# Kernel tuning notes

Measured on AMD Instinct MI355X. Metric: run time of the kernel, lower is better.

## Reference

```python
import jax, jax.numpy as jnp
import numpy as np
from jax import lax

SMOOTH = 1e-06
SKEL_ITERS = 10  # thresh_width in the original soft_skeletonize


def _maxpool3(x):
    # 3x3 max pool, stride 1, padding 1 on NCHW
    return lax.reduce_window(
        x, -jnp.inf, lax.max,
        window_dimensions=(1, 1, 3, 3),
        window_strides=(1, 1, 1, 1),
        padding=((0, 0), (0, 0), (1, 1), (1, 1)))


def soft_skeletonize(x):
    def body(i, x):
        min_pool_x = -_maxpool3(-x)                      # 3x3 min-pool (erosion)
        contour = jax.nn.relu(_maxpool3(min_pool_x) - min_pool_x)
        return jax.nn.relu(x - contour)
    return lax.fori_loop(0, SKEL_ITERS, body, x)


def norm_intersection(center_line, vessel):
    B, C = center_line.shape[:2]
    clf = center_line.reshape(B, C, -1)
    vf = vessel.reshape(B, C, -1)
    intersection = jnp.sum(clf * vf, axis=-1)
    return (intersection + SMOOTH) / (jnp.sum(clf, axis=-1) + SMOOTH)


def setup_inputs() -> dict:
    key = jax.random.key(0)
    k1, k2 = jax.random.split(key)
    B, C, H, W = 32, 1, 512, 512
    pred = jax.random.uniform(k1, (B, C, H, W), dtype=jnp.float32)
    target = (jax.random.uniform(k2, (B, C, H, W), dtype=jnp.float32) > 0.85).astype(jnp.float32)
    return {"pred": pred, "target": target}


def reference(pred, target):
    cl_pred = soft_skeletonize(pred)
    target_skeleton = soft_skeletonize(target)
    iflat = norm_intersection(cl_pred, target)
    tflat = norm_intersection(target_skeleton, pred)
    intersection = jnp.sum(iflat * tflat)
    return 1.0 - 2.0 * intersection / jnp.sum(iflat + tflat)
```

## Files before the change

kernel.cpp:

```cpp
#include <hip/hip_runtime.h>
#include <math.h>

#define HH 512
#define WW 512
#define BB 32
#define CHUNK 32

__device__ __forceinline__ float min3f(float a, float b, float c) {
    return fminf(fminf(a, b), c);
}
__device__ __forceinline__ float max3f(float a, float b, float c) {
    return fmaxf(fmaxf(a, b), c);
}
__device__ __forceinline__ float bf2f(unsigned short h) {
    return __uint_as_float((unsigned)h << 16);
}
__device__ __forceinline__ unsigned short f2bf(float f) {
    unsigned u = __float_as_uint(f);
    u += 0x7FFF + ((u >> 16) & 1);
    return (unsigned short)(u >> 16);
}

template <int F32>
__device__ __forceinline__ void loadrow12(const float* __restrict__ imgF,
                                          const unsigned short* __restrict__ imgH,
                                          int R, int cm4, int c0, int cp4,
                                          bool isL, bool isR, float* xr) {
    const int Rc = R < 0 ? 0 : (R > HH - 1 ? HH - 1 : R);
    if (F32) {
        const float* rb = imgF + (size_t)Rc * WW;
        float4 v0 = *(const float4*)(rb + cm4);
        float4 v1 = *(const float4*)(rb + c0);
        float4 v2 = *(const float4*)(rb + cp4);
        xr[0] = v0.x; xr[1] = v0.y; xr[2] = v0.z; xr[3] = v0.w;
        xr[4] = v1.x; xr[5] = v1.y; xr[6] = v1.z; xr[7] = v1.w;
        xr[8] = v2.x; xr[9] = v2.y; xr[10] = v2.z; xr[11] = v2.w;
    } else {
        const unsigned short* rb = imgH + (size_t)Rc * WW;
        ushort4 v0 = *(const ushort4*)(rb + cm4);
        ushort4 v1 = *(const ushort4*)(rb + c0);
        ushort4 v2 = *(const ushort4*)(rb + cp4);
        xr[0] = bf2f(v0.x); xr[1] = bf2f(v0.y); xr[2] = bf2f(v0.z); xr[3] = bf2f(v0.w);
        xr[4] = bf2f(v1.x); xr[5] = bf2f(v1.y); xr[6] = bf2f(v1.z); xr[7] = bf2f(v1.w);
        xr[8] = bf2f(v2.x); xr[9] = bf2f(v2.y); xr[10] = bf2f(v2.z); xr[11] = bf2f(v2.w);
    }
    if (isL) xr[3] = xr[0];
    if (isR) xr[8] = xr[7];
}

template <int SRCF32, int FUSED>
__device__ __forceinline__ void rowstep(
    const float* __restrict__ imgF, const unsigned short* __restrict__ imgH,
    const float* __restrict__ cmp, unsigned short* __restrict__ outp,
    float& acc0, float& acc1,
    int R, int cm4, int gx0, int cp4, bool isL, bool isR, bool doStore,
    float (&xA)[12], float (&xL)[12],
    float (&hm0o)[10], float (&hm0n)[10], float (&mn0p)[8],
    float (&hx0o)[8], float (&hx0n)[8],
    float (&x0o)[8], float (&x0n)[8],
    float (&hm1o)[6], float (&hm1n)[6], float (&mn1p)[4],
    float (&hx1o)[4], float (&hx1n)[4],
    float (&x1o)[4], float (&x1n)[4],
    float4& cqC, float4& cqL) {
    loadrow12<SRCF32>(imgF, imgH, R + 3, cm4, gx0, cp4, isL, isR, xL);

    float4 cmpCur;
    if (FUSED) {
        cmpCur = cqC;
        int Rc = R - 1;
        Rc = Rc < 0 ? 0 : (Rc > HH - 1 ? HH - 1 : Rc);
        cqL = *(const float4*)(cmp + (size_t)Rc * WW + gx0);
    }

    float hm0c[10];
    #pragma unroll
    for (int i = 0; i < 10; ++i) hm0c[i] = min3f(xA[i], xA[i + 1], xA[i + 2]);

    float mn0n[10];
    #pragma unroll
    for (int i = 0; i < 10; ++i) mn0n[i] = min3f(hm0o[i], hm0n[i], hm0c[i]);
    if (!((unsigned)(R - 1) < HH)) {
        #pragma unroll
        for (int i = 0; i < 10; ++i) mn0n[i] = -INFINITY;
    }
    if (isL) { mn0n[0] = -INFINITY; mn0n[1] = -INFINITY; mn0n[2] = -INFINITY; }
    if (isR) { mn0n[7] = -INFINITY; mn0n[8] = -INFINITY; mn0n[9] = -INFINITY; }

    float hx0c[8];
    #pragma unroll
    for (int j = 0; j < 8; ++j) hx0c[j] = max3f(mn0n[j], mn0n[j + 1], mn0n[j + 2]);

    float x1c[8];
    #pragma unroll
    for (int j = 0; j < 8; ++j) {
        float mp = max3f(hx0o[j], hx0n[j], hx0c[j]);
        float ct = fmaxf(mp - mn0p[j], 0.0f);
        x1c[j] = fmaxf(x0o[j] - ct, 0.0f);
    }
    if (!((unsigned)(R - 2) < HH)) {
        #pragma unroll
        for (int j = 0; j < 8; ++j) x1c[j] = INFINITY;
    }
    if (isL) { x1c[0] = INFINITY; x1c[1] = INFINITY; }
    if (isR) { x1c[6] = INFINITY; x1c[7] = INFINITY; }

    #pragma unroll
    for (int i = 0; i < 10; ++i) hm0o[i] = hm0c[i];
    #pragma unroll
    for (int j = 0; j < 8; ++j) { mn0p[j] = mn0n[j + 1]; hx0o[j] = hx0c[j]; x0o[j] = xA[j + 2]; }

    float hm1c[6];
    #pragma unroll
    for (int k = 0; k < 6; ++k) hm1c[k] = min3f(x1c[k], x1c[k + 1], x1c[k + 2]);

    float mn1n[6];
    #pragma unroll
    for (int k = 0; k < 6; ++k) mn1n[k] = min3f(hm1o[k], hm1n[k], hm1c[k]);
    if (!((unsigned)(R - 3) < HH)) {
        #pragma unroll
        for (int k = 0; k < 6; ++k) mn1n[k] = -INFINITY;
    }
    if (isL) mn1n[0] = -INFINITY;
    if (isR) mn1n[5] = -INFINITY;

    float hx1c[4];
    #pragma unroll
    for (int m = 0; m < 4; ++m) hx1c[m] = max3f(mn1n[m], mn1n[m + 1], mn1n[m + 2]);

    if (doStore) {
        float o[4];
        #pragma unroll
        for (int m = 0; m < 4; ++m) {
            float mp = max3f(hx1o[m], hx1n[m], hx1c[m]);
            float ct = fmaxf(mp - mn1p[m], 0.0f);
            o[m] = fmaxf(x1o[m] - ct, 0.0f);
        }
        if (FUSED) {
            acc0 += o[0] * cmpCur.x + o[1] * cmpCur.y + o[2] * cmpCur.z + o[3] * cmpCur.w;
            acc1 += o[0] + o[1] + o[2] + o[3];
        } else {
            ushort4 ov;
            ov.x = f2bf(o[0]); ov.y = f2bf(o[1]); ov.z = f2bf(o[2]); ov.w = f2bf(o[3]);
            *(ushort4*)(outp + (size_t)(R - 4) * WW + gx0) = ov;
        }
    }

    #pragma unroll
    for (int k = 0; k < 6; ++k) hm1o[k] = hm1c[k];
    #pragma unroll
    for (int m = 0; m < 4; ++m) { mn1p[m] = mn1n[m + 1]; hx1o[m] = hx1c[m]; x1o[m] = x1c[m + 2]; }
}

template <int SRCF32, int FUSED>
__global__ __launch_bounds__(256) void skel2b_t(const float* __restrict__ sfA,
                                                const float* __restrict__ sfB,
                                                const unsigned short* __restrict__ shA,
                                                const unsigned short* __restrict__ shB,
                                                const float* __restrict__ cmpA,
                                                const float* __restrict__ cmpB,
                                                unsigned short* __restrict__ dst,
                                                float* __restrict__ partials) {
    const int s = blockIdx.x * 64 + threadIdx.x;
    const int y0 = (blockIdx.y * 4 + threadIdx.y) * CHUNK;
    const int z = blockIdx.z;
    const float* imgF = nullptr;
    const unsigned short* imgH = nullptr;
    if (SRCF32) imgF = (z < BB) ? (sfA + (size_t)z * (HH * WW))
                                : (sfB + (size_t)(z - BB) * (HH * WW));
    else        imgH = (z < BB) ? (shA + (size_t)z * (HH * WW))
                                : (shB + (size_t)(z - BB) * (HH * WW));
    const float* cmp = nullptr;
    if (FUSED) cmp = (z < BB) ? (cmpA + (size_t)z * (HH * WW))
                              : (cmpB + (size_t)(z - BB) * (HH * WW));
    unsigned short* outp = FUSED ? nullptr : (dst + (size_t)z * (HH * WW));
    const int gx0 = 4 * s;
    const bool isL = (s == 0), isR = (s == 127);
    const int cm4 = isL ? 0 : gx0 - 4;
    const int cp4 = isR ? gx0 : gx0 + 4;

    float hm0a[10], hm0b[10], mn0p[8];
    float hx0a[8], hx0b[8], x0a[8], x0b[8];
    float hm1a[6], hm1b[6], mn1p[4];
    float hx1a[4], hx1b[4], x1a[4], x1b[4];
    float xs0[12], xs1[12], xs2[12], xs3[12];
    float4 cq0, cq1, cq2, cq3;

    #pragma unroll
    for (int i = 0; i < 10; ++i) { hm0a[i] = INFINITY; hm0b[i] = INFINITY; }
    #pragma unroll
    for (int j = 0; j < 8; ++j)  { mn0p[j] = -INFINITY; hx0a[j] = -INFINITY; hx0b[j] = -INFINITY; x0a[j] = INFINITY; x0b[j] = INFINITY; }
    #pragma unroll
    for (int k = 0; k < 6; ++k)  { hm1a[k] = INFINITY; hm1b[k] = INFINITY; }
    #pragma unroll
    for (int m = 0; m < 4; ++m)  { mn1p[m] = -INFINITY; hx1a[m] = -INFINITY; hx1b[m] = -INFINITY; x1a[m] = INFINITY; x1b[m] = INFINITY; }
    cq0.x = cq0.y = cq0.z = cq0.w = 0.f;
    cq1 = cq0; cq2 = cq0; cq3 = cq0;

    float acc0 = 0.0f, acc1 = 0.0f;

    loadrow12<SRCF32>(imgF, imgH, y0 - 4, cm4, gx0, cp4, isL, isR, xs0);
    loadrow12<SRCF32>(imgF, imgH, y0 - 3, cm4, gx0, cp4, isL, isR, xs1);
    loadrow12<SRCF32>(imgF, imgH, y0 - 2, cm4, gx0, cp4, isL, isR, xs2);

    #pragma unroll 1
    for (int it = 0; it < (CHUNK + 8) / 4; ++it) {
        const int Rb = y0 - 4 + 4 * it;
        const bool doStore = (it >= 2);
        rowstep<SRCF32, FUSED>(imgF, imgH, cmp, outp, acc0, acc1,
            Rb + 0, cm4, gx0, cp4, isL, isR, doStore,
            xs0, xs3, hm0a, hm0b, mn0p, hx0a, hx0b, x0a, x0b,
            hm1a, hm1b, mn1p, hx1a, hx1b, x1a, x1b, cq0, cq3);
        rowstep<SRCF32, FUSED>(imgF, imgH, cmp, outp, acc0, acc1,
            Rb + 1, cm4, gx0, cp4, isL, isR, doStore,
            xs1, xs0, hm0b, hm0a, mn0p, hx0b, hx0a, x0b, x0a,
            hm1b, hm1a, mn1p, hx1b, hx1a, x1b, x1a, cq1, cq0);
        rowstep<SRCF32, FUSED>(imgF, imgH, cmp, outp, acc0, acc1,
            Rb + 2, cm4, gx0, cp4, isL, isR, doStore,
            xs2, xs1, hm0a, hm0b, mn0p, hx0a, hx0b, x0a, x0b,
            hm1a, hm1b, mn1p, hx1a, hx1b, x1a, x1b, cq2, cq1);
        rowstep<SRCF32, FUSED>(imgF, imgH, cmp, outp, acc0, acc1,
            Rb + 3, cm4, gx0, cp4, isL, isR, doStore,
            xs3, xs2, hm0b, hm0a, mn0p, hx0b, hx0a, x0b, x0a,
            hm1b, hm1a, mn1p, hx1b, hx1a, x1b, x1a, cq3, cq2);
    }

    if (FUSED) {
        for (int off = 32; off; off >>= 1) {
            acc0 += __shfl_down(acc0, off);
            acc1 += __shfl_down(acc1, off);
        }
        __shared__ float red[4][2];
        if (threadIdx.x == 0) { red[threadIdx.y][0] = acc0; red[threadIdx.y][1] = acc1; }
        __syncthreads();
        if (threadIdx.x == 0 && threadIdx.y == 0) {
            const int tile = blockIdx.x * gridDim.y + blockIdx.y;
            float* p = partials + ((size_t)z * 16 + tile) * 2;
            p[0] = red[0][0] + red[1][0] + red[2][0] + red[3][0];
            p[1] = red[0][1] + red[1][1] + red[2][1] + red[3][1];
        }
    }
}

__global__ __launch_bounds__(64) void finalize2(const float* __restrict__ partials,
                                                int ntiles,
                                                float* __restrict__ out) {
    const int b = threadIdx.x;
    float iflat = 0.f, tflat = 0.f;
    if (b < BB) {
        float v0 = 0.f, v1 = 0.f, v2 = 0.f, v3 = 0.f;
        for (int t = 0; t < ntiles; ++t) {
            v0 += partials[((size_t)b * 16 + t) * 2 + 0];
            v1 += partials[((size_t)b * 16 + t) * 2 + 1];
            v2 += partials[((size_t)(b + BB) * 16 + t) * 2 + 0];
            v3 += partials[((size_t)(b + BB) * 16 + t) * 2 + 1];
        }
        iflat = (v0 + 1e-6f) / (v1 + 1e-6f);
        tflat = (v2 + 1e-6f) / (v3 + 1e-6f);
    }
    float prod = iflat * tflat;
    float ssum = iflat + tflat;
    for (int off = 32; off; off >>= 1) {
        prod += __shfl_down(prod, off);
        ssum += __shfl_down(ssum, off);
    }
    if (threadIdx.x == 0) out[0] = 1.0f - 2.0f * prod / ssum;
}

extern "C" void kernel_launch(void* const* d_in, const int* in_sizes, int n_in,
                              void* d_out, int out_size, void* d_ws, size_t ws_size,
                              hipStream_t stream) {
    const float* pred = (const float*)d_in[0];
    const float* target = (const float*)d_in[1];
    float* out = (float*)d_out;
    char* ws = (char*)d_ws;
    const size_t N = (size_t)HH * WW;
    const size_t HALF = (size_t)BB * N;
    const size_t IMG16 = HALF * sizeof(unsigned short);

    dim3 block(64, 4);
    const int nby = HH / (CHUNK * 4);
    const int ntiles = 2 * nby;

    if (ws_size >= 4 * IMG16 + (1 << 16)) {
        unsigned short* A = (unsigned short*)ws;
        unsigned short* B = (unsigned short*)(ws + 2 * IMG16);
        float* partials = (float*)(ws + 4 * IMG16);
        dim3 grid(2, nby, 2 * BB);
        skel2b_t<1, 0><<<grid, block, 0, stream>>>(pred, target, nullptr, nullptr,
                                                   nullptr, nullptr, A, nullptr);
        skel2b_t<0, 0><<<grid, block, 0, stream>>>(nullptr, nullptr, A, A + HALF,
                                                   nullptr, nullptr, B, nullptr);
        skel2b_t<0, 0><<<grid, block, 0, stream>>>(nullptr, nullptr, B, B + HALF,
                                                   nullptr, nullptr, A, nullptr);
        skel2b_t<0, 0><<<grid, block, 0, stream>>>(nullptr, nullptr, A, A + HALF,
                                                   nullptr, nullptr, B, nullptr);
        skel2b_t<0, 1><<<grid, block, 0, stream>>>(nullptr, nullptr, B, B + HALF,
                                                   target, pred, nullptr, partials);
        finalize2<<<1, 64, 0, stream>>>(partials, ntiles, out);
    } else {
        unsigned short* b0 = (unsigned short*)ws;
        unsigned short* b1 = (unsigned short*)(ws + IMG16);
        float* partials = (float*)(ws + 2 * IMG16);
        dim3 grid(2, nby, BB);
        skel2b_t<1, 0><<<grid, block, 0, stream>>>(pred, pred, nullptr, nullptr,
                                                   nullptr, nullptr, b0, nullptr);
        skel2b_t<0, 0><<<grid, block, 0, stream>>>(nullptr, nullptr, b0, b0,
                                                   nullptr, nullptr, b1, nullptr);
        skel2b_t<0, 0><<<grid, block, 0, stream>>>(nullptr, nullptr, b1, b1,
                                                   nullptr, nullptr, b0, nullptr);
        skel2b_t<0, 0><<<grid, block, 0, stream>>>(nullptr, nullptr, b0, b0,
                                                   nullptr, nullptr, b1, nullptr);
        skel2b_t<0, 1><<<grid, block, 0, stream>>>(nullptr, nullptr, b1, b1,
                                                   target, target, nullptr, partials);
        skel2b_t<1, 0><<<grid, block, 0, stream>>>(target, target, nullptr, nullptr,
                                                   nullptr, nullptr, b0, nullptr);
        skel2b_t<0, 0><<<grid, block, 0, stream>>>(nullptr, nullptr, b0, b0,
                                                   nullptr, nullptr, b1, nullptr);
        skel2b_t<0, 0><<<grid, block, 0, stream>>>(nullptr, nullptr, b1, b1,
                                                   nullptr, nullptr, b0, nullptr);
        skel2b_t<0, 0><<<grid, block, 0, stream>>>(nullptr, nullptr, b0, b0,
                                                   nullptr, nullptr, b1, nullptr);
        skel2b_t<0, 1><<<grid, block, 0, stream>>>(nullptr, nullptr, b1, b1,
                                                   pred, pred, nullptr,
                                                   partials + (size_t)BB * 16 * 2);
        finalize2<<<1, 64, 0, stream>>>(partials, ntiles, out);
    }
}
```

Before: 141.2 us.

## Switch skeleton pipeline to packed fp16 math and halve row chunk size

Intermediate skeleton images and in-register stencil values move from bf16 storage with fp32 math to packed half2 values, processed with v_pk_min/max/add_f16 inline asm. Neighbour columns are formed with alignbit shifts, and border handling uses precomputed mask words instead of per-element branches. The aim is to halve ALU instruction count and register pressure for the erosion/dilation chain. CHUNK also drops from 32 to 16, which doubles the grid rows, raises halo recompute overhead and changes the launch configuration. fp16 gives different rounding and range than bf16/fp32 and could shift results.

```diff
diff --git a/kernel.cpp b/kernel.cpp
--- a/kernel.cpp
+++ b/kernel.cpp
@@ -1,51 +1,66 @@
 #include <hip/hip_runtime.h>
+#include <hip/hip_fp16.h>
 #include <math.h>
 
 #define HH 512
 #define WW 512
 #define BB 32
-#define CHUNK 32
-
-__device__ __forceinline__ float min3f(float a, float b, float c) {
-    return fminf(fminf(a, b), c);
-}
-__device__ __forceinline__ float max3f(float a, float b, float c) {
-    return fmaxf(fmaxf(a, b), c);
-}
-__device__ __forceinline__ float bf2f(unsigned short h) {
-    return __uint_as_float((unsigned)h << 16);
-}
-__device__ __forceinline__ unsigned short f2bf(float f) {
-    unsigned u = __float_as_uint(f);
-    u += 0x7FFF + ((u >> 16) & 1);
-    return (unsigned short)(u >> 16);
+#define CHUNK 16
+
+typedef unsigned u32;
+
+#define NEG_INF2 0xFC00FC00u
+#define POS_INF2 0x7C007C00u
+
+__device__ __forceinline__ u32 pkmin(u32 a, u32 b) {
+    u32 r; asm("v_pk_min_f16 %0, %1, %2" : "=v"(r) : "v"(a), "v"(b)); return r;
+}
+__device__ __forceinline__ u32 pkmax(u32 a, u32 b) {
+    u32 r; asm("v_pk_max_f16 %0, %1, %2" : "=v"(r) : "v"(a), "v"(b)); return r;
+}
+__device__ __forceinline__ u32 pksub(u32 a, u32 b) {
+    u32 r; asm("v_pk_add_f16 %0, %1, %2 neg_lo:[0,1] neg_hi:[0,1]" : "=v"(r) : "v"(a), "v"(b)); return r;
+}
+__device__ __forceinline__ u32 min3p(u32 a, u32 b, u32 c) { return pkmin(pkmin(a, b), c); }
+__device__ __forceinline__ u32 max3p(u32 a, u32 b, u32 c) { return pkmax(pkmax(a, b), c); }
+
+__device__ __forceinline__ u32 shl1(u32 a, u32 b) {
+    return __builtin_amdgcn_alignbit(b, a, 16);
+}
+
+union H2U { __half2 h; u32 u; };
+__device__ __forceinline__ u32 f2toh2(float lo, float hi) {
+    H2U t; t.h = __float22half2_rn(make_float2(lo, hi)); return t.u;
+}
+__device__ __forceinline__ float2 h2tof2(u32 v) {
+    H2U t; t.u = v; return __half22float2(t.h);
 }
 
 template <int F32>
-__device__ __forceinline__ void loadrow12(const float* __restrict__ imgF,
-                                          const unsigned short* __restrict__ imgH,
-                                          int R, int cm4, int c0, int cp4,
-                                          bool isL, bool isR, float* xr) {
+__device__ __forceinline__ void loadrow6(const float* __restrict__ imgF,
+                                         const unsigned short* __restrict__ imgH,
+                                         int R, int cm4, int c0, int cp4,
+                                         bool isL, bool isR, u32* X) {
     const int Rc = R < 0 ? 0 : (R > HH - 1 ? HH - 1 : R);
     if (F32) {
         const float* rb = imgF + (size_t)Rc * WW;
         float4 v0 = *(const float4*)(rb + cm4);
         float4 v1 = *(const float4*)(rb + c0);
         float4 v2 = *(const float4*)(rb + cp4);
-        xr[0] = v0.x; xr[1] = v0.y; xr[2] = v0.z; xr[3] = v0.w;
-        xr[4] = v1.x; xr[5] = v1.y; xr[6] = v1.z; xr[7] = v1.w;
-        xr[8] = v2.x; xr[9] = v2.y; xr[10] = v2.z; xr[11] = v2.w;
+        X[0] = f2toh2(v0.x, v0.y); X[1] = f2toh2(v0.z, v0.w);
+        X[2] = f2toh2(v1.x, v1.y); X[3] = f2toh2(v1.z, v1.w);
+        X[4] = f2toh2(v2.x, v2.y); X[5] = f2toh2(v2.z, v2.w);
     } else {
         const unsigned short* rb = imgH + (size_t)Rc * WW;
-        ushort4 v0 = *(const ushort4*)(rb + cm4);
-        ushort4 v1 = *(const ushort4*)(rb + c0);
-        ushort4 v2 = *(const ushort4*)(rb + cp4);
-        xr[0] = bf2f(v0.x); xr[1] = bf2f(v0.y); xr[2] = bf2f(v0.z); xr[3] = bf2f(v0.w);
-        xr[4] = bf2f(v1.x); xr[5] = bf2f(v1.y); xr[6] = bf2f(v1.z); xr[7] = bf2f(v1.w);
-        xr[8] = bf2f(v2.x); xr[9] = bf2f(v2.y); xr[10] = bf2f(v2.z); xr[11] = bf2f(v2.w);
-    }
-    if (isL) xr[3] = xr[0];
-    if (isR) xr[8] = xr[7];
+        uint2 a = *(const uint2*)(rb + cm4);
+        uint2 b = *(const uint2*)(rb + c0);
+        uint2 c = *(const uint2*)(rb + cp4);
+        X[0] = a.x; X[1] = a.y; X[2] = b.x; X[3] = b.y; X[4] = c.x; X[5] = c.y;
+    }
+    u32 fl = __builtin_amdgcn_perm(X[0], X[1], 0x05040100u);
+    X[1] = isL ? fl : X[1];
+    u32 fr = __builtin_amdgcn_perm(X[4], X[3], 0x07060302u);
+    X[4] = isR ? fr : X[4];
 }
 
 template <int SRCF32, int FUSED>
@@ -54,15 +69,16 @@
     const float* __restrict__ cmp, unsigned short* __restrict__ outp,
     float& acc0, float& acc1,
     int R, int cm4, int gx0, int cp4, bool isL, bool isR, bool doStore,
-    float (&xA)[12], float (&xL)[12],
-    float (&hm0o)[10], float (&hm0n)[10], float (&mn0p)[8],
-    float (&hx0o)[8], float (&hx0n)[8],
-    float (&x0o)[8], float (&x0n)[8],
-    float (&hm1o)[6], float (&hm1n)[6], float (&mn1p)[4],
-    float (&hx1o)[4], float (&hx1n)[4],
-    float (&x1o)[4], float (&x1n)[4],
+    u32 (&X)[6], u32 (&XL)[6],
+    u32 (&hm0o)[6], u32 (&hm0n)[6], u32 (&mn0p)[4],
+    u32 (&hx0o)[4], u32 (&hx0n)[4],
+    u32 (&x0o)[4], u32 (&x0n)[4],
+    u32 (&hm1o)[4], u32 (&hm1n)[4], u32 (&mn1p)[2],
+    u32 (&hx1o)[2], u32 (&hx1n)[2],
+    u32 (&x1o)[2], u32 (&x1n)[2],
+    const u32 (&mk)[8],
     float4& cqC, float4& cqL) {
-    loadrow12<SRCF32>(imgF, imgH, R + 3, cm4, gx0, cp4, isL, isR, xL);
+    loadrow6<SRCF32>(imgF, imgH, R + 3, cm4, gx0, cp4, isL, isR, XL);
 
     float4 cmpCur;
     if (FUSED) {
@@ -72,87 +88,106 @@
         cqL = *(const float4*)(cmp + (size_t)Rc * WW + gx0);
     }
 
-    float hm0c[10];
-    #pragma unroll
-    for (int i = 0; i < 10; ++i) hm0c[i] = min3f(xA[i], xA[i + 1], xA[i + 2]);
-
-    float mn0n[10];
-    #pragma unroll
-    for (int i = 0; i < 10; ++i) mn0n[i] = min3f(hm0o[i], hm0n[i], hm0c[i]);
+    u32 L[7];
+    L[0] = shl1(X[0], X[0]);
+    #pragma unroll
+    for (int j = 1; j <= 5; ++j) L[j] = shl1(X[j - 1], X[j]);
+    L[6] = shl1(X[5], X[5]);
+    u32 hm0c[6];
+    #pragma unroll
+    for (int j = 0; j < 6; ++j) hm0c[j] = min3p(L[j], X[j], L[j + 1]);
+
+    u32 M[6];
+    #pragma unroll
+    for (int j = 0; j < 6; ++j) M[j] = min3p(hm0o[j], hm0n[j], hm0c[j]);
     if (!((unsigned)(R - 1) < HH)) {
         #pragma unroll
-        for (int i = 0; i < 10; ++i) mn0n[i] = -INFINITY;
-    }
-    if (isL) { mn0n[0] = -INFINITY; mn0n[1] = -INFINITY; mn0n[2] = -INFINITY; }
-    if (isR) { mn0n[7] = -INFINITY; mn0n[8] = -INFINITY; mn0n[9] = -INFINITY; }
-
-    float hx0c[8];
-    #pragma unroll
-    for (int j = 0; j < 8; ++j) hx0c[j] = max3f(mn0n[j], mn0n[j + 1], mn0n[j + 2]);
-
-    float x1c[8];
-    #pragma unroll
-    for (int j = 0; j < 8; ++j) {
-        float mp = max3f(hx0o[j], hx0n[j], hx0c[j]);
-        float ct = fmaxf(mp - mn0p[j], 0.0f);
-        x1c[j] = fmaxf(x0o[j] - ct, 0.0f);
+        for (int j = 0; j < 6; ++j) M[j] = NEG_INF2;
+    }
+    M[0] = pkmin(M[0], mk[0]); M[1] = pkmin(M[1], mk[1]);
+    M[4] = pkmin(M[4], mk[2]); M[5] = pkmin(M[5], mk[3]);
+
+    u32 ML[6];
+    #pragma unroll
+    for (int j = 1; j <= 5; ++j) ML[j] = shl1(M[j - 1], M[j]);
+    u32 hx0c[4];
+    #pragma unroll
+    for (int j = 0; j < 4; ++j) hx0c[j] = max3p(ML[j + 1], M[j + 1], ML[j + 2]);
+
+    u32 x1c[4];
+    #pragma unroll
+    for (int j = 0; j < 4; ++j) {
+        u32 mp = max3p(hx0o[j], hx0n[j], hx0c[j]);
+        u32 ct = pkmax(pksub(mp, mn0p[j]), 0u);
+        x1c[j] = pkmax(pksub(x0o[j], ct), 0u);
     }
     if (!((unsigned)(R - 2) < HH)) {
         #pragma unroll
-        for (int j = 0; j < 8; ++j) x1c[j] = INFINITY;
-    }
-    if (isL) { x1c[0] = INFINITY; x1c[1] = INFINITY; }
-    if (isR) { x1c[6] = INFINITY; x1c[7] = INFINITY; }
-
-    #pragma unroll
-    for (int i = 0; i < 10; ++i) hm0o[i] = hm0c[i];
-    #pragma unroll
-    for (int j = 0; j < 8; ++j) { mn0p[j] = mn0n[j + 1]; hx0o[j] = hx0c[j]; x0o[j] = xA[j + 2]; }
-
-    float hm1c[6];
-    #pragma unroll
-    for (int k = 0; k < 6; ++k) hm1c[k] = min3f(x1c[k], x1c[k + 1], x1c[k + 2]);
-
-    float mn1n[6];
-    #pragma unroll
-    for (int k = 0; k < 6; ++k) mn1n[k] = min3f(hm1o[k], hm1n[k], hm1c[k]);
+        for (int j = 0; j < 4; ++j) x1c[j] = POS_INF2;
+    }
+    x1c[0] = pkmax(x1c[0], mk[4]);
+    x1c[3] = pkmax(x1c[3], mk[5]);
+
+    #pragma unroll
+    for (int j = 0; j < 6; ++j) hm0o[j] = hm0c[j];
+    #pragma unroll
+    for (int j = 0; j < 4; ++j) { mn0p[j] = M[j + 1]; hx0o[j] = hx0c[j]; x0o[j] = X[j + 1]; }
+
+    u32 XL1[5];
+    XL1[0] = shl1(x1c[0], x1c[0]);
+    #pragma unroll
+    for (int j = 1; j <= 3; ++j) XL1[j] = shl1(x1c[j - 1], x1c[j]);
+    XL1[4] = shl1(x1c[3], x1c[3]);
+    u32 hm1c[4];
+    #pragma unroll
+    for (int j = 0; j < 4; ++j) hm1c[j] = min3p(XL1[j], x1c[j], XL1[j + 1]);
+
+    u32 M1[4];
+    #pragma unroll
+    for (int j = 0; j < 4; ++j) M1[j] = min3p(hm1o[j], hm1n[j], hm1c[j]);
     if (!((unsigned)(R - 3) < HH)) {
         #pragma unroll
-        for (int k = 0; k < 6; ++k) mn1n[k] = -INFINITY;
-    }
-    if (isL) mn1n[0] = -INFINITY;
-    if (isR) mn1n[5] = -INFINITY;
-
-    float hx1c[4];
-    #pragma unroll
-    for (int m = 0; m < 4; ++m) hx1c[m] = max3f(mn1n[m], mn1n[m + 1], mn1n[m + 2]);
+        for (int j = 0; j < 4; ++j) M1[j] = NEG_INF2;
+    }
+    M1[0] = pkmin(M1[0], mk[6]);
+    M1[3] = pkmin(M1[3], mk[7]);
+
+    u32 M1s[4];
+    #pragma unroll
+    for (int j = 1; j <= 3; ++j) M1s[j] = shl1(M1[j - 1], M1[j]);
+    u32 hx1c[2];
+    hx1c[0] = max3p(M1s[1], M1[1], M1s[2]);
+    hx1c[1] = max3p(M1s[2], M1[2], M1s[3]);
 
     if (doStore) {
-        float o[4];
+        u32 o[2];
         #pragma unroll
-        for (int m = 0; m < 4; ++m) {
-            float mp = max3f(hx1o[m], hx1n[m], hx1c[m]);
-            float ct = fmaxf(mp - mn1p[m], 0.0f);
-            o[m] = fmaxf(x1o[m] - ct, 0.0f);
+        for (int k = 0; k < 2; ++k) {
+            u32 mp = max3p(hx1o[k], hx1n[k], hx1c[k]);
+            u32 ct = pkmax(pksub(mp, mn1p[k]), 0u);
+            o[k] = pkmax(pksub(x1o[k], ct), 0u);
         }
         if (FUSED) {
-            acc0 += o[0] * cmpCur.x + o[1] * cmpCur.y + o[2] * cmpCur.z + o[3] * cmpCur.w;
-            acc1 += o[0] + o[1] + o[2] + o[3];
+            float2 f0 = h2tof2(o[0]);
+            float2 f1 = h2tof2(o[1]);
+            acc0 += f0.x * cmpCur.x + f0.y * cmpCur.y + f1.x * cmpCur.z + f1.y * cmpCur.w;
+            acc1 += f0.x + f0.y + f1.x + f1.y;
         } else {
-            ushort4 ov;
-            ov.x = f2bf(o[0]); ov.y = f2bf(o[1]); ov.z = f2bf(o[2]); ov.w = f2bf(o[3]);
-            *(ushort4*)(outp + (size_t)(R - 4) * WW + gx0) = ov;
-        }
-    }
-
-    #pragma unroll
-    for (int k = 0; k < 6; ++k) hm1o[k] = hm1c[k];
-    #pragma unroll
-    for (int m = 0; m < 4; ++m) { mn1p[m] = mn1n[m + 1]; hx1o[m] = hx1c[m]; x1o[m] = x1c[m + 2]; }
+            uint2 ov;
+            ov.x = o[0]; ov.y = o[1];
+            *(uint2*)(outp + (size_t)(R - 4) * WW + gx0) = ov;
+        }
+    }
+
+    #pragma unroll
+    for (int j = 0; j < 4; ++j) hm1o[j] = hm1c[j];
+    mn1p[0] = M1[1]; mn1p[1] = M1[2];
+    hx1o[0] = hx1c[0]; hx1o[1] = hx1c[1];
+    x1o[0] = x1c[1]; x1o[1] = x1c[2];
 }
 
 template <int SRCF32, int FUSED>
-__global__ __launch_bounds__(256) void skel2b_t(const float* __restrict__ sfA,
+__global__ __launch_bounds__(256) void skel2h_t(const float* __restrict__ sfA,
                                                 const float* __restrict__ sfB,
                                                 const unsigned short* __restrict__ shA,
                                                 const unsigned short* __restrict__ shB,
@@ -178,29 +213,44 @@
     const int cm4 = isL ? 0 : gx0 - 4;
     const int cp4 = isR ? gx0 : gx0 + 4;
 
-    float hm0a[10], hm0b[10], mn0p[8];
-    float hx0a[8], hx0b[8], x0a[8], x0b[8];
-    float hm1a[6], hm1b[6], mn1p[4];
-    float hx1a[4], hx1b[4], x1a[4], x1b[4];
-    float xs0[12], xs1[12], xs2[12], xs3[12];
+    u32 mk[8];
+    mk[0] = isL ? 0xFC007C00u : POS_INF2;
+    mk[1] = isL ? NEG_INF2    : POS_INF2;
+    mk[2] = isR ? NEG_INF2    : POS_INF2;
+    mk[3] = isR ? 0x7C00FC00u : POS_INF2;
+    mk[4] = isL ? POS_INF2    : NEG_INF2;
+    mk[5] = isR ? POS_INF2    : NEG_INF2;
+    mk[6] = isL ? 0xFC007C00u : POS_INF2;
+    mk[7] = isR ? 0x7C00FC00u : POS_INF2;
+
+    u32 hm0a[6], hm0b[6], mn0p[4];
+    u32 hx0a[4], hx0b[4], x0a[4], x0b[4];
+    u32 hm1a[4], hm1b[4], mn1p[2];
+    u32 hx1a[2], hx1b[2], x1a[2], x1b[2];
+    u32 xs0[6], xs1[6], xs2[6], xs3[6];
     float4 cq0, cq1, cq2, cq3;
 
     #pragma unroll
-    for (int i = 0; i < 10; ++i) { hm0a[i] = INFINITY; hm0b[i] = INFINITY; }
-    #pragma unroll
-    for (int j = 0; j < 8; ++j)  { mn0p[j] = -INFINITY; hx0a[j] = -INFINITY; hx0b[j] = -INFINITY; x0a[j] = INFINITY; x0b[j] = INFINITY; }
-    #pragma unroll
-    for (int k = 0; k < 6; ++k)  { hm1a[k] = INFINITY; hm1b[k] = INFINITY; }
-    #pragma unroll
-    for (int m = 0; m < 4; ++m)  { mn1p[m] = -INFINITY; hx1a[m] = -INFINITY; hx1b[m] = -INFINITY; x1a[m] = INFINITY; x1b[m] = INFINITY; }
+    for (int j = 0; j < 6; ++j) { hm0a[j] = POS_INF2; hm0b[j] = POS_INF2; }
+    #pragma unroll
+    for (int j = 0; j < 4; ++j) {
+        mn0p[j] = NEG_INF2; hx0a[j] = NEG_INF2; hx0b[j] = NEG_INF2;
+        x0a[j] = POS_INF2; x0b[j] = POS_INF2;
+        hm1a[j] = POS_INF2; hm1b[j] = POS_INF2;
+    }
+    #pragma unroll
+    for (int k = 0; k < 2; ++k) {
+        mn1p[k] = NEG_INF2; hx1a[k] = NEG_INF2; hx1b[k] = NEG_INF2;
+        x1a[k] = POS_INF2; x1b[k] = POS_INF2;
+    }
     cq0.x = cq0.y = cq0.z = cq0.w = 0.f;
     cq1 = cq0; cq2 = cq0; cq3 = cq0;
 
     float acc0 = 0.0f, acc1 = 0.0f;
 
-    loadrow12<SRCF32>(imgF, imgH, y0 - 4, cm4, gx0, cp4, isL, isR, xs0);
-    loadrow12<SRCF32>(imgF, imgH, y0 - 3, cm4, gx0, cp4, isL, isR, xs1);
-    loadrow12<SRCF32>(imgF, imgH, y0 - 2, cm4, gx0, cp4, isL, isR, xs2);
+    loadrow6<SRCF32>(imgF, imgH, y0 - 4, cm4, gx0, cp4, isL, isR, xs0);
+    loadrow6<SRCF32>(imgF, imgH, y0 - 3, cm4, gx0, cp4, isL, isR, xs1);
+    loadrow6<SRCF32>(imgF, imgH, y0 - 2, cm4, gx0, cp4, isL, isR, xs2);
 
     #pragma unroll 1
     for (int it = 0; it < (CHUNK + 8) / 4; ++it) {
@@ -209,19 +259,19 @@
         rowstep<SRCF32, FUSED>(imgF, imgH, cmp, outp, acc0, acc1,
             Rb + 0, cm4, gx0, cp4, isL, isR, doStore,
             xs0, xs3, hm0a, hm0b, mn0p, hx0a, hx0b, x0a, x0b,
-            hm1a, hm1b, mn1p, hx1a, hx1b, x1a, x1b, cq0, cq3);
+            hm1a, hm1b, mn1p, hx1a, hx1b, x1a, x1b, mk, cq0, cq3);
         rowstep<SRCF32, FUSED>(imgF, imgH, cmp, outp, acc0, acc1,
             Rb + 1, cm4, gx0, cp4, isL, isR, doStore,
             xs1, xs0, hm0b, hm0a, mn0p, hx0b, hx0a, x0b, x0a,
-            hm1b, hm1a, mn1p, hx1b, hx1a, x1b, x1a, cq1, cq0);
+            hm1b, hm1a, mn1p, hx1b, hx1a, x1b, x1a, mk, cq1, cq0);
         rowstep<SRCF32, FUSED>(imgF, imgH, cmp, outp, acc0, acc1,
             Rb + 2, cm4, gx0, cp4, isL, isR, doStore,
             xs2, xs1, hm0a, hm0b, mn0p, hx0a, hx0b, x0a, x0b,
-            hm1a, hm1b, mn1p, hx1a, hx1b, x1a, x1b, cq2, cq1);
+            hm1a, hm1b, mn1p, hx1a, hx1b, x1a, x1b, mk, cq2, cq1);
         rowstep<SRCF32, FUSED>(imgF, imgH, cmp, outp, acc0, acc1,
             Rb + 3, cm4, gx0, cp4, isL, isR, doStore,
             xs3, xs2, hm0b, hm0a, mn0p, hx0b, hx0a, x0b, x0a,
-            hm1b, hm1a, mn1p, hx1b, hx1a, x1b, x1a, cq3, cq2);
+            hm1b, hm1a, mn1p, hx1b, hx1a, x1b, x1a, mk, cq3, cq2);
     }
 
     if (FUSED) {
@@ -286,15 +336,15 @@
         unsigned short* B = (unsigned short*)(ws + 2 * IMG16);
         float* partials = (float*)(ws + 4 * IMG16);
         dim3 grid(2, nby, 2 * BB);
-        skel2b_t<1, 0><<<grid, block, 0, stream>>>(pred, target, nullptr, nullptr,
+        skel2h_t<1, 0><<<grid, block, 0, stream>>>(pred, target, nullptr, nullptr,
                                                    nullptr, nullptr, A, nullptr);
-        skel2b_t<0, 0><<<grid, block, 0, stream>>>(nullptr, nullptr, A, A + HALF,
+        skel2h_t<0, 0><<<grid, block, 0, stream>>>(nullptr, nullptr, A, A + HALF,
                                                    nullptr, nullptr, B, nullptr);
-        skel2b_t<0, 0><<<grid, block, 0, stream>>>(nullptr, nullptr, B, B + HALF,
+        skel2h_t<0, 0><<<grid, block, 0, stream>>>(nullptr, nullptr, B, B + HALF,
                                                    nullptr, nullptr, A, nullptr);
-        skel2b_t<0, 0><<<grid, block, 0, stream>>>(nullptr, nullptr, A, A + HALF,
+        skel2h_t<0, 0><<<grid, block, 0, stream>>>(nullptr, nullptr, A, A + HALF,
                                                    nullptr, nullptr, B, nullptr);
-        skel2b_t<0, 1><<<grid, block, 0, stream>>>(nullptr, nullptr, B, B + HALF,
+        skel2h_t<0, 1><<<grid, block, 0, stream>>>(nullptr, nullptr, B, B + HALF,
                                                    target, pred, nullptr, partials);
         finalize2<<<1, 64, 0, stream>>>(partials, ntiles, out);
     } else {
@@ -302,25 +352,25 @@
         unsigned short* b1 = (unsigned short*)(ws + IMG16);
         float* partials = (float*)(ws + 2 * IMG16);
         dim3 grid(2, nby, BB);
-        skel2b_t<1, 0><<<grid, block, 0, stream>>>(pred, pred, nullptr, nullptr,
+        skel2h_t<1, 0><<<grid, block, 0, stream>>>(pred, pred, nullptr, nullptr,
                                                    nullptr, nullptr, b0, nullptr);
-        skel2b_t<0, 0><<<grid, block, 0, stream>>>(nullptr, nullptr, b0, b0,
+        skel2h_t<0, 0><<<grid, block, 0, stream>>>(nullptr, nullptr, b0, b0,
                                                    nullptr, nullptr, b1, nullptr);
-        skel2b_t<0, 0><<<grid, block, 0, stream>>>(nullptr, nullptr, b1, b1,
+        skel2h_t<0, 0><<<grid, block, 0, stream>>>(nullptr, nullptr, b1, b1,
                                                    nullptr, nullptr, b0, nullptr);
-        skel2b_t<0, 0><<<grid, block, 0, stream>>>(nullptr, nullptr, b0, b0,
+        skel2h_t<0, 0><<<grid, block, 0, stream>>>(nullptr, nullptr, b0, b0,
                                                    nullptr, nullptr, b1, nullptr);
-        skel2b_t<0, 1><<<grid, block, 0, stream>>>(nullptr, nullptr, b1, b1,
+        skel2h_t<0, 1><<<grid, block, 0, stream>>>(nullptr, nullptr, b1, b1,
                                                    target, target, nullptr, partials);
-        skel2b_t<1, 0><<<grid, block, 0, stream>>>(target, target, nullptr, nullptr,
+        skel2h_t<1, 0><<<grid, block, 0, stream>>>(target, target, nullptr, nullptr,
                                                    nullptr, nullptr, b0, nullptr);
-        skel2b_t<0, 0><<<grid, block, 0, stream>>>(nullptr, nullptr, b0, b0,
+        skel2h_t<0, 0><<<grid, block, 0, stream>>>(nullptr, nullptr, b0, b0,
                                                    nullptr, nullptr, b1, nullptr);
-        skel2b_t<0, 0><<<grid, block, 0, stream>>>(nullptr, nullptr, b1, b1,
+        skel2h_t<0, 0><<<grid, block, 0, stream>>>(nullptr, nullptr, b1, b1,
                                                    nullptr, nullptr, b0, nullptr);
-        skel2b_t<0, 0><<<grid, block, 0, stream>>>(nullptr, nullptr, b0, b0,
+        skel2h_t<0, 0><<<grid, block, 0, stream>>>(nullptr, nullptr, b0, b0,
                                                    nullptr, nullptr, b1, nullptr);
-        skel2b_t<0, 1><<<grid, block, 0, stream>>>(nullptr, nullptr, b1, b1,
+        skel2h_t<0, 1><<<grid, block, 0, stream>>>(nullptr, nullptr, b1, b1,
                                                    pred, pred, nullptr,
                                                    partials + (size_t)BB * 16 * 2);
         finalize2<<<1, 64, 0, stream>>>(partials, ntiles, out);
```

Result: slower. 156.5 us (+10.8%).
